# Kernel tuning notes

Hardware: AMD Instinct MI355X
Metric: run time of the kernel (lower is better)

Reference implementation:

```python
import jax, jax.numpy as jnp
import numpy as np

SIZES = [(64, 32), (32, 16), (16, 8), (8, 16), (16, 32)]
BZ, T, D = 2048, 512, 64


def setup_inputs() -> dict:
    key = jax.random.key(0)
    ks = jax.random.split(key, 32)
    inp = {
        "X": jax.random.normal(ks[0], (BZ, T, D), jnp.float32),
        "missing_mask": (jax.random.uniform(ks[1], (BZ, T, D)) < 0.8).astype(jnp.float32),
        "imputation_latent": jax.random.normal(ks[2], (BZ, T, D), jnp.float32),
    }
    for i, (din, dh) in enumerate(SIZES):
        s = 1.0 / np.sqrt(dh)  # PyTorch RNNCell init range
        k = 3 + 4 * i
        inp[f"wih{i}"] = jax.random.uniform(ks[k], (3 * dh, din), jnp.float32, -s, s)
        inp[f"whh{i}"] = jax.random.uniform(ks[k + 1], (3 * dh, dh), jnp.float32, -s, s)
        inp[f"bih{i}"] = jax.random.uniform(ks[k + 2], (3 * dh,), jnp.float32, -s, s)
        inp[f"bhh{i}"] = jax.random.uniform(ks[k + 3], (3 * dh,), jnp.float32, -s, s)
    so = 1.0 / np.sqrt(32)
    inp["out_w"] = jax.random.uniform(ks[23], (D, 32), jnp.float32, -so, so)
    inp["out_b"] = jax.random.uniform(ks[24], (D,), jnp.float32, -so, so)
    return inp


def _gru_cell(x, h, wih, whh, bih, bhh):
    # PyTorch nn.GRUCell gate order: r, z, n
    gi = x @ wih.T + bih
    gh = h @ whh.T + bhh
    ir, iz, inn = jnp.split(gi, 3, axis=-1)
    hr, hz, hn = jnp.split(gh, 3, axis=-1)
    r = jax.nn.sigmoid(ir + hr)
    z = jax.nn.sigmoid(iz + hz)
    n = jnp.tanh(inn + r * hn)
    return (1.0 - z) * n + z * h


def _forward(X, missing_mask, imputation_latent, params, out_w, out_b):
    imputed = X * missing_mask + imputation_latent * (1.0 - missing_mask)
    xs = jnp.swapaxes(imputed, 0, 1)  # [T, B, D]
    bz = X.shape[0]
    h0 = tuple(jnp.zeros((bz, dh), X.dtype) for _, dh in SIZES)

    def step(hs, x):
        new = []
        inp_x = x
        for i, (wih, whh, bih, bhh) in enumerate(params):
            h = _gru_cell(inp_x, hs[i], wih, whh, bih, bhh)
            new.append(h)
            inp_x = h  # layer i+1 consumes the freshly-updated hidden state
        return tuple(new), new[-1]

    _, hcol = jax.lax.scan(step, h0, xs)  # [T, B, 32]
    hcol = jnp.swapaxes(hcol, 0, 1)  # [B, T, 32]
    return hcol @ out_w.T + out_b


def reference(X, missing_mask, imputation_latent,
              wih0, whh0, bih0, bhh0, wih1, whh1, bih1, bhh1,
              wih2, whh2, bih2, bhh2, wih3, whh3, bih3, bhh3,
              wih4, whh4, bih4, bhh4, out_w, out_b):
    params = [(wih0, whh0, bih0, bhh0), (wih1, whh1, bih1, bhh1),
              (wih2, whh2, bih2, bhh2), (wih3, whh3, bih3, bhh3),
              (wih4, whh4, bih4, bhh4)]
    return _forward(X, missing_mask, imputation_latent, params, out_w, out_b)
```

## Files before the change

kernel.cpp:

```cpp
#include <hip/hip_runtime.h>

typedef short s16x8 __attribute__((ext_vector_type(8)));
typedef short s16x4 __attribute__((ext_vector_type(4)));
typedef float f32x4 __attribute__((ext_vector_type(4)));
typedef unsigned int u32;
typedef unsigned short u16;

#define NT 512
#define DD 64
#define BB 8
#define NTH 512

#define CHUNK 1024

#define P2STRIDE (5*CHUNK)
#define PH0 0
#define PH1 CHUNK
#define PH2 (2*CHUNK)
#define PH3 (3*CHUNK)
#define PH4 (4*CHUNK)
#define FRTOT2 (2*P2STRIDE)
#define NSTEP2 518

#define PSTRIDE (7*CHUNK)
#define XIN0 0
#define H0C (2*CHUNK)
#define H1C (3*CHUNK)
#define H2C (4*CHUNK)
#define H3C (5*CHUNK)
#define H4C (6*CHUNK)
#define FRTOT (2*PSTRIDE)
#define NSTEP_FB 517

#define MFMA16(A,B,C) __builtin_amdgcn_mfma_f32_16x16x32_bf16(A,B,C,0,0,0)

__device__ __forceinline__ float sigf(float x){ return 1.0f/(1.0f+__expf(-x)); }
__device__ __forceinline__ float tanhf2(float x){ return 2.0f/(1.0f+__expf(-2.0f*x)) - 1.0f; }

__device__ __forceinline__ u16 f2bf(float f) {
  u32 u = __builtin_bit_cast(u32, f);
  return (u16)((u + 0x7fffu + ((u >> 16) & 1u)) >> 16);
}
__device__ __forceinline__ float bf2f(u16 h) {
  u32 u = ((u32)h) << 16;
  return __builtin_bit_cast(float, u);
}

__device__ __forceinline__ void load_wfrag(const float* __restrict__ W, int row0, int nrow, int din,
                                           int kbase, int lane, s16x8& hi, s16x8& lo)
{
  const int m = lane & 15, kb = lane >> 4;
#pragma unroll
  for (int e = 0; e < 8; ++e) {
    int k = kbase + kb*8 + e;
    float v = (m < nrow && k < din) ? W[(size_t)(row0 + m)*din + k] : 0.0f;
    u16 h = f2bf(v);
    hi[e] = (short)h;
    lo[e] = (short)f2bf(v - bf2f(h));
  }
}

__device__ __forceinline__ void read_b(const u16* base, int lane, s16x8& hi, s16x8& lo)
{
  const int off = ((lane >> 4) << 8) + ((lane & 15) << 3);
  hi = *(const s16x8*)(base + off);
  lo = *(const s16x8*)(base + off + 128);
}

__device__ __forceinline__ void combine_write(
    f32x4 aR, f32x4 aZ, f32x4 aNi, f32x4 aNh,
    float (&hprev)[4], u16* hdst_base, int jbase, int nrow, int lane)
{
  const int bb = lane & 15, q = lane >> 4;
  float hv[4];
#pragma unroll
  for (int i = 0; i < 4; ++i) {
    float rr = sigf(aR[i]);
    float zz = sigf(aZ[i]);
    float nn = tanhf2(aNi[i] + rr*aNh[i]);
    hv[i] = (1.0f - zz)*nn + zz*hprev[i];
    hprev[i] = hv[i];
  }
  if (bb < 8 && q*4 < nrow) {
    const int j = jbase + q*4;
    const int kb = j >> 3, e = j & 7;
    s16x4 hh, ll;
#pragma unroll
    for (int i = 0; i < 4; ++i) {
      u16 h = f2bf(hv[i]);
      hh[i] = (short)h;
      ll[i] = (short)f2bf(hv[i] - bf2f(h));
    }
    u16* dst = hdst_base + kb*256 + bb*8 + e;
    *(s16x4*)dst = hh;
    *(s16x4*)(dst + 128) = ll;
  }
}

__global__ __launch_bounds__(256)
void gi0_gemm(const float* __restrict__ X, const float* __restrict__ M, const float* __restrict__ L,
              const float* __restrict__ wih0, const float* __restrict__ bih0,
              float* __restrict__ gi)
{
  __shared__ u32 xs[128*65];
  const int tid = threadIdx.x;
  const int wv = tid >> 6, lane = tid & 63;
  const int q = lane >> 4;
  const int b = blockIdx.x >> 2;
  const int t0 = (blockIdx.x & 3) * 128;
  const size_t base = ((size_t)b*NT + t0)*DD;

  for (int i = tid; i < 128*64; i += 256) {
    const int t = i >> 6, d = i & 63;
    float x = X[base+i], m = M[base+i], l = L[base+i];
    float v = x*m + l*(1.0f - m);
    u16 h = f2bf(v);
    u16 lo2 = f2bf(v - bf2f(h));
    xs[t*65 + d] = (u32)h | ((u32)lo2 << 16);
  }

  s16x8 Ah[6][2], Al[6][2];
  f32x4 cb[6];
#pragma unroll
  for (int tile = 0; tile < 6; ++tile) {
#pragma unroll
    for (int c = 0; c < 2; ++c)
      load_wfrag(wih0, tile*16, 16, 64, c*32, lane, Ah[tile][c], Al[tile][c]);
#pragma unroll
    for (int i = 0; i < 4; ++i) cb[tile][i] = bih0[tile*16 + q*4 + i];
  }
  __syncthreads();

#pragma unroll
  for (int g2 = 0; g2 < 2; ++g2) {
    const int tloc = g2*64 + wv*16 + (lane & 15);
    s16x8 Bh[2], Bl[2];
#pragma unroll
    for (int c = 0; c < 2; ++c) {
      const u32* p = &xs[tloc*65 + c*32 + q*8];
#pragma unroll
      for (int e = 0; e < 8; ++e) {
        u32 v = p[e];
        Bh[c][e] = (short)(v & 0xffffu);
        Bl[c][e] = (short)(v >> 16);
      }
    }
    float* gp = gi + ((size_t)b*NT + t0 + tloc)*96 + q*4;
#pragma unroll
    for (int tile = 0; tile < 6; ++tile) {
      f32x4 acc = cb[tile];
#pragma unroll
      for (int c = 0; c < 2; ++c) {
        acc = MFMA16(Ah[tile][c], Bh[c], acc);
        acc = MFMA16(Ah[tile][c], Bl[c], acc);
        acc = MFMA16(Al[tile][c], Bh[c], acc);
      }
      *(f32x4*)(gp + tile*16) = acc;
    }
  }
}

__device__ __forceinline__ void wave_l0(
    const float* __restrict__ Whh, const float* __restrict__ bhh,
    const float* __restrict__ gi, int jbase,
    u16* FRu, float* OST, float* __restrict__ out, int b0, int w, int lane)
{
  s16x8 Ahh[3], Ahl[3];
#pragma unroll
  for (int g = 0; g < 3; ++g)
    load_wfrag(Whh, g*32 + jbase, 16, 32, 0, lane, Ahh[g], Ahl[g]);
  const int q = lane >> 4;
  f32x4 cRh, cZh, cNh;
#pragma unroll
  for (int i = 0; i < 4; ++i) {
    int j = jbase + q*4 + i;
    cRh[i] = bhh[j]; cZh[i] = bhh[32+j]; cNh[i] = bhh[64+j];
  }
  float hprev[4] = {0.f,0.f,0.f,0.f};

  const size_t grow = (size_t)(b0 + (lane & 7)) * ((size_t)NT*96);
  f32x4 gR, gZ, gN;
  {
    const float* p = gi + grow + jbase + q*4;
    gR = *(const f32x4*)(p); gZ = *(const f32x4*)(p+32); gN = *(const f32x4*)(p+64);
  }
  for (int s = 0; s < NSTEP2; ++s) {
    const int par = s & 1, rp = par ^ 1;
    f32x4 nR, nZ, nN;
    if (s < 511) {
      const float* p = gi + grow + (size_t)(s+1)*96 + jbase + q*4;
      nR = *(const f32x4*)(p); nZ = *(const f32x4*)(p+32); nN = *(const f32x4*)(p+64);
    }
    if (s <= 511) {
      f32x4 aR = gR + cRh, aZ = gZ + cZh, aNi = gN, aNh = cNh;
      s16x8 bh_, bl_;
      read_b(FRu + rp*P2STRIDE + PH0, lane, bh_, bl_);
      aR  = MFMA16(Ahh[0], bh_, aR);  aR  = MFMA16(Ahh[0], bl_, aR);  aR  = MFMA16(Ahl[0], bh_, aR);
      aZ  = MFMA16(Ahh[1], bh_, aZ);  aZ  = MFMA16(Ahh[1], bl_, aZ);  aZ  = MFMA16(Ahl[1], bh_, aZ);
      aNh = MFMA16(Ahh[2], bh_, aNh); aNh = MFMA16(Ahh[2], bl_, aNh); aNh = MFMA16(Ahl[2], bh_, aNh);
      combine_write(aR, aZ, aNi, aNh, hprev, FRu + par*P2STRIDE + PH0, jbase, 16, lane);
    }
    if (s >= 6)
      out[((size_t)(b0 + w)*NT + (s-6))*DD + lane] = OST[rp*520 + w*65 + lane];
    gR = nR; gZ = nZ; gN = nN;
    __syncthreads();
  }
}

template<int DIN, int DH>
__device__ __forceinline__ void wave_mid(
    const float* __restrict__ Wih, const float* __restrict__ Whh,
    const float* __restrict__ bih, const float* __restrict__ bhh,
    int jbase, int xc, int hc, int s0, int s1,
    u16* FRu, float* OST, float* __restrict__ out, int b0, int w, int lane)
{
  const int nrow = (DH - jbase) < 16 ? (DH - jbase) : 16;
  s16x8 Axh[3], Axl[3], Ahh[3], Ahl[3];
#pragma unroll
  for (int g = 0; g < 3; ++g) {
    load_wfrag(Wih, g*DH + jbase, nrow, DIN, 0, lane, Axh[g], Axl[g]);
    load_wfrag(Whh, g*DH + jbase, nrow, DH, 0, lane, Ahh[g], Ahl[g]);
  }
  const int q = lane >> 4;
  f32x4 cR, cZ, cNi, cNh;
#pragma unroll
  for (int i = 0; i < 4; ++i) {
    int lr = q*4 + i;
    int j = jbase + lr;
    bool jr = lr < nrow;
    cR[i]  = jr ? bih[j] + bhh[j] : 0.f;
    cZ[i]  = jr ? bih[DH+j] + bhh[DH+j] : 0.f;
    cNi[i] = jr ? bih[2*DH+j] : 0.f;
    cNh[i] = jr ? bhh[2*DH+j] : 0.f;
  }
  float hprev[4] = {0.f,0.f,0.f,0.f};

  for (int s = 0; s < NSTEP2; ++s) {
    const int par = s & 1, rp = par ^ 1;
    if (s >= s0 && s <= s1) {
      f32x4 aR = cR, aZ = cZ, aNi = cNi, aNh = cNh;
      s16x8 bh_, bl_;
      read_b(FRu + rp*P2STRIDE + xc, lane, bh_, bl_);
      aR  = MFMA16(Axh[0], bh_, aR);  aR  = MFMA16(Axh[0], bl_, aR);  aR  = MFMA16(Axl[0], bh_, aR);
      aZ  = MFMA16(Axh[1], bh_, aZ);  aZ  = MFMA16(Axh[1], bl_, aZ);  aZ  = MFMA16(Axl[1], bh_, aZ);
      aNi = MFMA16(Axh[2], bh_, aNi); aNi = MFMA16(Axh[2], bl_, aNi); aNi = MFMA16(Axl[2], bh_, aNi);
      read_b(FRu + rp*P2STRIDE + hc, lane, bh_, bl_);
      aR  = MFMA16(Ahh[0], bh_, aR);  aR  = MFMA16(Ahh[0], bl_, aR);  aR  = MFMA16(Ahl[0], bh_, aR);
      aZ  = MFMA16(Ahh[1], bh_, aZ);  aZ  = MFMA16(Ahh[1], bl_, aZ);  aZ  = MFMA16(Ahl[1], bh_, aZ);
      aNh = MFMA16(Ahh[2], bh_, aNh); aNh = MFMA16(Ahh[2], bl_, aNh); aNh = MFMA16(Ahl[2], bh_, aNh);
      combine_write(aR, aZ, aNi, aNh, hprev, FRu + par*P2STRIDE + hc, jbase, nrow, lane);
    }
    if (s >= 6)
      out[((size_t)(b0 + w)*NT + (s-6))*DD + lane] = OST[rp*520 + w*65 + lane];
    __syncthreads();
  }
}

__device__ __forceinline__ void wave_out2(
    const float* __restrict__ OW, const float* __restrict__ OBb,
    u16* FRu, float* OST, float* __restrict__ out, int b0, int w, int lane)
{
  s16x8 Oh[4], Ol[4];
  f32x4 cO[4];
  const int q = lane >> 4;
#pragma unroll
  for (int t4 = 0; t4 < 4; ++t4) {
    load_wfrag(OW, t4*16, 16, 32, 0, lane, Oh[t4], Ol[t4]);
#pragma unroll
    for (int i = 0; i < 4; ++i) cO[t4][i] = OBb[t4*16 + q*4 + i];
  }
  for (int s = 0; s < NSTEP2; ++s) {
    const int par = s & 1, rp = par ^ 1;
    if (s >= 5 && s <= 516) {
      s16x8 bh_, bl_;
      read_b(FRu + rp*P2STRIDE + PH4, lane, bh_, bl_);
      const int bb = lane & 15;
#pragma unroll
      for (int t4 = 0; t4 < 4; ++t4) {
        f32x4 a_ = cO[t4];
        a_ = MFMA16(Oh[t4], bh_, a_); a_ = MFMA16(Oh[t4], bl_, a_); a_ = MFMA16(Ol[t4], bh_, a_);
        if (bb < 8) {
#pragma unroll
          for (int i = 0; i < 4; ++i) OST[par*520 + bb*65 + t4*16 + q*4 + i] = a_[i];
        }
      }
    }
    if (s >= 6)
      out[((size_t)(b0 + w)*NT + (s-6))*DD + lane] = OST[rp*520 + w*65 + lane];
    __syncthreads();
  }
}

__global__ __launch_bounds__(NTH, 1)
void gru_rec(const float* __restrict__ gi,
             const float* __restrict__ whh0, const float* __restrict__ bhh0,
             const float* __restrict__ wih1, const float* __restrict__ whh1, const float* __restrict__ bih1, const float* __restrict__ bhh1,
             const float* __restrict__ wih2, const float* __restrict__ whh2, const float* __restrict__ bih2, const float* __restrict__ bhh2,
             const float* __restrict__ wih3, const float* __restrict__ whh3, const float* __restrict__ bih3, const float* __restrict__ bhh3,
             const float* __restrict__ wih4, const float* __restrict__ whh4, const float* __restrict__ bih4, const float* __restrict__ bhh4,
             const float* __restrict__ out_w, const float* __restrict__ out_b,
             float* __restrict__ out)
{
  __shared__ __align__(16) u16 FRu[FRTOT2];
  __shared__ float OST[2*520];
  const int tid = threadIdx.x;
  const int w = tid >> 6, lane = tid & 63;
  const int b0 = blockIdx.x * BB;

  for (int i = tid; i < FRTOT2; i += NTH) FRu[i] = 0;
  for (int i = tid; i < 2*520; i += NTH) OST[i] = 0.f;
  __syncthreads();

  if (w == 0)
    wave_l0(whh0, bhh0, gi,  0, FRu, OST, out, b0, w, lane);
  else if (w == 1)
    wave_l0(whh0, bhh0, gi, 16, FRu, OST, out, b0, w, lane);
  else if (w == 2)
    wave_mid<32,16>(wih1,whh1,bih1,bhh1,  0, PH0, PH1, 1, 512, FRu, OST, out, b0, w, lane);
  else if (w == 4)
    wave_mid<16, 8>(wih2,whh2,bih2,bhh2,  0, PH1, PH2, 2, 513, FRu, OST, out, b0, w, lane);
  else if (w == 5)
    wave_mid< 8,16>(wih3,whh3,bih3,bhh3,  0, PH2, PH3, 3, 514, FRu, OST, out, b0, w, lane);
  else if (w == 3)
    wave_mid<16,32>(wih4,whh4,bih4,bhh4,  0, PH3, PH4, 4, 515, FRu, OST, out, b0, w, lane);
  else if (w == 6)
    wave_mid<16,32>(wih4,whh4,bih4,bhh4, 16, PH3, PH4, 4, 515, FRu, OST, out, b0, w, lane);
  else
    wave_out2(out_w, out_b, FRu, OST, out, b0, w, lane);
}

__device__ __forceinline__ void write_x(u16* FRu, int par, int w, int lane, float v)
{
  const int d = lane;
  const int chunk = d >> 5, kb = (d >> 3) & 3, e = d & 7;
  u16 h = f2bf(v);
  u16 l2 = f2bf(v - bf2f(h));
  u16* p = FRu + par*PSTRIDE + XIN0 + chunk*CHUNK + kb*256 + w*8 + e;
  p[0] = h; p[128] = l2;
}

template<int DIN, int DH, int NXC>
__device__ __forceinline__ void wave_gru_fb(
    const float* __restrict__ Wih, const float* __restrict__ Whh,
    const float* __restrict__ bih, const float* __restrict__ bhh,
    int jbase, int xc, int hc, int s0, int s1,
    u16* FRu, float* OST,
    const float* __restrict__ X, const float* __restrict__ Mm, const float* __restrict__ Ll,
    float* __restrict__ out, int b0, int w, int lane)
{
  const int nrow = (DH - jbase) < 16 ? (DH - jbase) : 16;
  s16x8 Axh[3][NXC], Axl[3][NXC], Ahh[3], Ahl[3];
#pragma unroll
  for (int g = 0; g < 3; ++g) {
#pragma unroll
    for (int c = 0; c < NXC; ++c)
      load_wfrag(Wih, g*DH + jbase, nrow, DIN, c*32, lane, Axh[g][c], Axl[g][c]);
    load_wfrag(Whh, g*DH + jbase, nrow, DH, 0, lane, Ahh[g], Ahl[g]);
  }
  f32x4 cR, cZ, cNi, cNh;
  {
    const int q = lane >> 4;
#pragma unroll
    for (int i = 0; i < 4; ++i) {
      int lr = q*4 + i;
      int j = jbase + lr;
      bool jr = lr < nrow;
      cR[i]  = jr ? bih[j] + bhh[j] : 0.f;
      cZ[i]  = jr ? bih[DH+j] + bhh[DH+j] : 0.f;
      cNi[i] = jr ? bih[2*DH+j] : 0.f;
      cNh[i] = jr ? bhh[2*DH+j] : 0.f;
    }
  }
  float hprev[4] = {0.f, 0.f, 0.f, 0.f};

  const size_t gbase = ((size_t)(b0 + w))*((size_t)NT*DD) + lane;
  float rx = X[gbase], rm = Mm[gbase], rl = Ll[gbase];
  write_x(FRu, 1, w, lane, rx*rm + rl*(1.0f - rm));
  rx = X[gbase + DD]; rm = Mm[gbase + DD]; rl = Ll[gbase + DD];
  __syncthreads();

  for (int s = 0; s < NSTEP_FB; ++s) {
    const int par = s & 1, rp = par ^ 1;
    float nx = 0.f, nm = 0.f, nl = 0.f;
    if (s <= 509) {
      size_t g = gbase + (size_t)(s+2)*DD;
      nx = X[g]; nm = Mm[g]; nl = Ll[g];
    }
    f32x4 aR = cR, aZ = cZ, aNi = cNi, aNh = cNh;
    const bool run = (s >= s0) && (s <= s1);
    if (run) {
      const u16* RB = FRu + rp*PSTRIDE;
      s16x8 bh_, bl_;
#pragma unroll
      for (int c = 0; c < NXC; ++c) {
        read_b(RB + xc + c*CHUNK, lane, bh_, bl_);
        aR  = MFMA16(Axh[0][c], bh_, aR);  aR  = MFMA16(Axh[0][c], bl_, aR);  aR  = MFMA16(Axl[0][c], bh_, aR);
        aZ  = MFMA16(Axh[1][c], bh_, aZ);  aZ  = MFMA16(Axh[1][c], bl_, aZ);  aZ  = MFMA16(Axl[1][c], bh_, aZ);
        aNi = MFMA16(Axh[2][c], bh_, aNi); aNi = MFMA16(Axh[2][c], bl_, aNi); aNi = MFMA16(Axl[2][c], bh_, aNi);
      }
      read_b(RB + hc, lane, bh_, bl_);
      aR  = MFMA16(Ahh[0], bh_, aR);  aR  = MFMA16(Ahh[0], bl_, aR);  aR  = MFMA16(Ahl[0], bh_, aR);
      aZ  = MFMA16(Ahh[1], bh_, aZ);  aZ  = MFMA16(Ahh[1], bl_, aZ);  aZ  = MFMA16(Ahl[1], bh_, aZ);
      aNh = MFMA16(Ahh[2], bh_, aNh); aNh = MFMA16(Ahh[2], bl_, aNh); aNh = MFMA16(Ahl[2], bh_, aNh);
    }
    __syncthreads();

    if (run)
      combine_write(aR, aZ, aNi, aNh, hprev, FRu + par*PSTRIDE + hc, jbase, nrow, lane);
    if (s >= 5)
      out[((size_t)(b0 + w)*NT + (s-5))*DD + lane] = OST[w*65 + lane];
    if (s <= 510) write_x(FRu, par, w, lane, rx*rm + rl*(1.0f - rm));
    rx = nx; rm = nm; rl = nl;
    __syncthreads();
  }
}

__device__ __forceinline__ void wave_out_fb(
    const float* __restrict__ OW, const float* __restrict__ OBb,
    u16* FRu, float* OST,
    const float* __restrict__ X, const float* __restrict__ Mm, const float* __restrict__ Ll,
    float* __restrict__ out, int b0, int w, int lane)
{
  s16x8 Oh[4], Ol[4];
  f32x4 cO[4];
#pragma unroll
  for (int t4 = 0; t4 < 4; ++t4) {
    load_wfrag(OW, t4*16, 16, 32, 0, lane, Oh[t4], Ol[t4]);
#pragma unroll
    for (int i = 0; i < 4; ++i) cO[t4][i] = OBb[t4*16 + (lane>>4)*4 + i];
  }
  const size_t gbase = ((size_t)(b0 + w))*((size_t)NT*DD) + lane;
  float rx = X[gbase], rm = Mm[gbase], rl = Ll[gbase];
  write_x(FRu, 1, w, lane, rx*rm + rl*(1.0f - rm));
  rx = X[gbase + DD]; rm = Mm[gbase + DD]; rl = Ll[gbase + DD];
  __syncthreads();

  for (int s = 0; s < NSTEP_FB; ++s) {
    const int par = s & 1, rp = par ^ 1;
    float nx = 0.f, nm = 0.f, nl = 0.f;
    if (s <= 509) { size_t g = gbase + (size_t)(s+2)*DD; nx = X[g]; nm = Mm[g]; nl = Ll[g]; }
    if (s >= 5) {
      s16x8 bh_, bl_;
      read_b(FRu + rp*PSTRIDE + H4C, lane, bh_, bl_);
      const int bb = lane & 15, q = lane >> 4;
#pragma unroll
      for (int t4 = 0; t4 < 4; ++t4) {
        f32x4 a_ = cO[t4];
        a_ = MFMA16(Oh[t4], bh_, a_); a_ = MFMA16(Oh[t4], bl_, a_); a_ = MFMA16(Ol[t4], bh_, a_);
        if (bb < 8) {
#pragma unroll
          for (int i = 0; i < 4; ++i) OST[bb*65 + t4*16 + q*4 + i] = a_[i];
        }
      }
    }
    __syncthreads();
    if (s >= 5)
      out[((size_t)(b0 + w)*NT + (s-5))*DD + lane] = OST[w*65 + lane];
    if (s <= 510) write_x(FRu, par, w, lane, rx*rm + rl*(1.0f - rm));
    rx = nx; rm = nm; rl = nl;
    __syncthreads();
  }
}

__global__ __launch_bounds__(NTH, 1)
void gru_mfma(const float* __restrict__ X, const float* __restrict__ M, const float* __restrict__ L,
              const float* __restrict__ wih0, const float* __restrict__ whh0, const float* __restrict__ bih0, const float* __restrict__ bhh0,
              const float* __restrict__ wih1, const float* __restrict__ whh1, const float* __restrict__ bih1, const float* __restrict__ bhh1,
              const float* __restrict__ wih2, const float* __restrict__ whh2, const float* __restrict__ bih2, const float* __restrict__ bhh2,
              const float* __restrict__ wih3, const float* __restrict__ whh3, const float* __restrict__ bih3, const float* __restrict__ bhh3,
              const float* __restrict__ wih4, const float* __restrict__ whh4, const float* __restrict__ bih4, const float* __restrict__ bhh4,
              const float* __restrict__ out_w, const float* __restrict__ out_b,
              float* __restrict__ out)
{
  __shared__ __align__(16) u16 FRu[FRTOT];
  __shared__ float OST[8*65];
  const int tid = threadIdx.x;
  const int w = tid >> 6, lane = tid & 63;
  const int b0 = blockIdx.x * BB;

  for (int i = tid; i < FRTOT; i += NTH) FRu[i] = 0;
  for (int i = tid; i < 8*65; i += NTH) OST[i] = 0.f;
  __syncthreads();

  if (w == 0)
    wave_gru_fb<64,32,2>(wih0,whh0,bih0,bhh0,  0, XIN0, H0C, 0, 511, FRu, OST, X,M,L, out, b0, w, lane);
  else if (w == 1)
    wave_gru_fb<64,32,2>(wih0,whh0,bih0,bhh0, 16, XIN0, H0C, 0, 511, FRu, OST, X,M,L, out, b0, w, lane);
  else if (w == 2)
    wave_gru_fb<32,16,1>(wih1,whh1,bih1,bhh1,  0, H0C,  H1C, 1, 512, FRu, OST, X,M,L, out, b0, w, lane);
  else if (w == 4)
    wave_gru_fb<16, 8,1>(wih2,whh2,bih2,bhh2,  0, H1C,  H2C, 2, 513, FRu, OST, X,M,L, out, b0, w, lane);
  else if (w == 5)
    wave_gru_fb< 8,16,1>(wih3,whh3,bih3,bhh3,  0, H2C,  H3C, 3, 514, FRu, OST, X,M,L, out, b0, w, lane);
  else if (w == 3)
    wave_gru_fb<16,32,1>(wih4,whh4,bih4,bhh4,  0, H3C,  H4C, 4, 515, FRu, OST, X,M,L, out, b0, w, lane);
  else if (w == 6)
    wave_gru_fb<16,32,1>(wih4,whh4,bih4,bhh4, 16, H3C,  H4C, 4, 515, FRu, OST, X,M,L, out, b0, w, lane);
  else
    wave_out_fb(out_w, out_b, FRu, OST, X,M,L, out, b0, w, lane);
}

extern "C" void kernel_launch(void* const* d_in, const int* in_sizes, int n_in,
                              void* d_out, int out_size, void* d_ws, size_t ws_size,
                              hipStream_t stream)
{
  const float* X  = (const float*)d_in[0];
  const float* M  = (const float*)d_in[1];
  const float* L  = (const float*)d_in[2];
  const float* wp[20];
  for (int i = 0; i < 20; ++i) wp[i] = (const float*)d_in[3 + i];
  const float* ow = (const float*)d_in[23];
  const float* ob = (const float*)d_in[24];
  float* out = (float*)d_out;

  const size_t gi_bytes = (size_t)2048 * NT * 96 * sizeof(float);
  if (ws_size >= gi_bytes) {
    float* gi = (float*)d_ws;
    gi0_gemm<<<dim3(2048*4), dim3(256), 0, stream>>>(X, M, L, wp[0], wp[2], gi);
    gru_rec<<<dim3(2048 / BB), dim3(NTH), 0, stream>>>(
        gi, wp[1], wp[3],
        wp[4], wp[5], wp[6], wp[7],
        wp[8], wp[9], wp[10], wp[11],
        wp[12], wp[13], wp[14], wp[15],
        wp[16], wp[17], wp[18], wp[19],
        ow, ob, out);
  } else {
    gru_mfma<<<dim3(2048 / BB), dim3(NTH), 0, stream>>>(
        X, M, L,
        wp[0], wp[1], wp[2], wp[3],
        wp[4], wp[5], wp[6], wp[7],
        wp[8], wp[9], wp[10], wp[11],
        wp[12], wp[13], wp[14], wp[15],
        wp[16], wp[17], wp[18], wp[19],
        ow, ob, out);
  }
}
```

Before: 976.6 us.

## Write output directly from output wave, use lighter barrier, prefetch gi two steps

The recurrent kernel's output wave now writes its MFMA results straight to global memory, so the shared OST staging buffer and the per-step copy-out that every wave did are gone. __syncthreads is replaced by a barrier that waits only on LDS counters, so global loads and stores stay in flight across steps. Layer-0 gi loads are prefetched two steps ahead, and the r/z hidden biases are folded into the gi GEMM. bf16 hi/lo splitting now uses a packed convert instruction, and the step count drops by one. The main risk is memory ordering under the weaker barrier and differences in how the packed convert rounds.

```diff
diff --git a/kernel.cpp b/kernel.cpp
--- a/kernel.cpp
+++ b/kernel.cpp
@@ -20,7 +20,7 @@
 #define PH3 (3*CHUNK)
 #define PH4 (4*CHUNK)
 #define FRTOT2 (2*P2STRIDE)
-#define NSTEP2 518
+#define NSTEP2 517
 
 #define PSTRIDE (7*CHUNK)
 #define XIN0 0
@@ -46,6 +46,18 @@
   return __builtin_bit_cast(float, u);
 }
 
+__device__ __forceinline__ void soft_barrier() {
+  asm volatile("s_waitcnt lgkmcnt(0)" ::: "memory");
+  __builtin_amdgcn_s_barrier();
+  asm volatile("" ::: "memory");
+}
+
+__device__ __forceinline__ u32 cvtpk_bf16(float a, float b) {
+  u32 r;
+  asm("v_cvt_pk_bf16_f32 %0, %1, %2" : "=v"(r) : "v"(a), "v"(b));
+  return r;
+}
+
 __device__ __forceinline__ void load_wfrag(const float* __restrict__ W, int row0, int nrow, int din,
                                            int kbase, int lane, s16x8& hi, s16x8& lo)
 {
@@ -67,7 +79,7 @@
   lo = *(const s16x8*)(base + off + 128);
 }
 
-__device__ __forceinline__ void combine_write(
+__device__ __forceinline__ void combine_write2(
     f32x4 aR, f32x4 aZ, f32x4 aNi, f32x4 aNh,
     float (&hprev)[4], u16* hdst_base, int jbase, int nrow, int lane)
 {
@@ -83,6 +95,38 @@
   }
   if (bb < 8 && q*4 < nrow) {
     const int j = jbase + q*4;
+    u16* dst = hdst_base + ((j >> 3) << 8) + bb*8 + (j & 7);
+    u32 p01 = cvtpk_bf16(hv[0], hv[1]);
+    u32 p23 = cvtpk_bf16(hv[2], hv[3]);
+    float h0 = __builtin_bit_cast(float, p01 << 16);
+    float h1 = __builtin_bit_cast(float, p01 & 0xffff0000u);
+    float h2 = __builtin_bit_cast(float, p23 << 16);
+    float h3 = __builtin_bit_cast(float, p23 & 0xffff0000u);
+    u32 q01 = cvtpk_bf16(hv[0]-h0, hv[1]-h1);
+    u32 q23 = cvtpk_bf16(hv[2]-h2, hv[3]-h3);
+    uint2 hp_; hp_.x = p01; hp_.y = p23;
+    uint2 lp_; lp_.x = q01; lp_.y = q23;
+    *(uint2*)dst = hp_;
+    *(uint2*)(dst + 128) = lp_;
+  }
+}
+
+__device__ __forceinline__ void combine_write(
+    f32x4 aR, f32x4 aZ, f32x4 aNi, f32x4 aNh,
+    float (&hprev)[4], u16* hdst_base, int jbase, int nrow, int lane)
+{
+  const int bb = lane & 15, q = lane >> 4;
+  float hv[4];
+#pragma unroll
+  for (int i = 0; i < 4; ++i) {
+    float rr = sigf(aR[i]);
+    float zz = sigf(aZ[i]);
+    float nn = tanhf2(aNi[i] + rr*aNh[i]);
+    hv[i] = (1.0f - zz)*nn + zz*hprev[i];
+    hprev[i] = hv[i];
+  }
+  if (bb < 8 && q*4 < nrow) {
+    const int j = jbase + q*4;
     const int kb = j >> 3, e = j & 7;
     s16x4 hh, ll;
 #pragma unroll
@@ -100,6 +144,7 @@
 __global__ __launch_bounds__(256)
 void gi0_gemm(const float* __restrict__ X, const float* __restrict__ M, const float* __restrict__ L,
               const float* __restrict__ wih0, const float* __restrict__ bih0,
+              const float* __restrict__ bhh0,
               float* __restrict__ gi)
 {
   __shared__ u32 xs[128*65];
@@ -111,11 +156,11 @@
   const size_t base = ((size_t)b*NT + t0)*DD;
 
   for (int i = tid; i < 128*64; i += 256) {
-    const int t = i >> 6, d = i & 63;
     float x = X[base+i], m = M[base+i], l = L[base+i];
     float v = x*m + l*(1.0f - m);
     u16 h = f2bf(v);
     u16 lo2 = f2bf(v - bf2f(h));
+    const int t = i >> 6, d = i & 63;
     xs[t*65 + d] = (u32)h | ((u32)lo2 << 16);
   }
 
@@ -127,7 +172,12 @@
     for (int c = 0; c < 2; ++c)
       load_wfrag(wih0, tile*16, 16, 64, c*32, lane, Ah[tile][c], Al[tile][c]);
 #pragma unroll
-    for (int i = 0; i < 4; ++i) cb[tile][i] = bih0[tile*16 + q*4 + i];
+    for (int i = 0; i < 4; ++i) {
+      int row = tile*16 + q*4 + i;
+      float bv = bih0[row];
+      if (tile < 4) bv += bhh0[row];
+      cb[tile][i] = bv;
+    }
   }
   __syncthreads();
 
@@ -163,47 +213,41 @@
 __device__ __forceinline__ void wave_l0(
     const float* __restrict__ Whh, const float* __restrict__ bhh,
     const float* __restrict__ gi, int jbase,
-    u16* FRu, float* OST, float* __restrict__ out, int b0, int w, int lane)
+    u16* FRu, int b0, int lane)
 {
   s16x8 Ahh[3], Ahl[3];
 #pragma unroll
   for (int g = 0; g < 3; ++g)
     load_wfrag(Whh, g*32 + jbase, 16, 32, 0, lane, Ahh[g], Ahl[g]);
   const int q = lane >> 4;
-  f32x4 cRh, cZh, cNh;
-#pragma unroll
-  for (int i = 0; i < 4; ++i) {
-    int j = jbase + q*4 + i;
-    cRh[i] = bhh[j]; cZh[i] = bhh[32+j]; cNh[i] = bhh[64+j];
-  }
+  f32x4 cNh;
+#pragma unroll
+  for (int i = 0; i < 4; ++i) cNh[i] = bhh[64 + jbase + q*4 + i];
   float hprev[4] = {0.f,0.f,0.f,0.f};
 
-  const size_t grow = (size_t)(b0 + (lane & 7)) * ((size_t)NT*96);
-  f32x4 gR, gZ, gN;
-  {
-    const float* p = gi + grow + jbase + q*4;
-    gR = *(const f32x4*)(p); gZ = *(const f32x4*)(p+32); gN = *(const f32x4*)(p+64);
-  }
+  const float* gp = gi + (size_t)(b0 + (lane & 7)) * ((size_t)NT*96) + jbase + q*4;
+  f32x4 gR0, gZ0, gN0, gR1, gZ1, gN1;
+  gR0 = *(const f32x4*)(gp); gZ0 = *(const f32x4*)(gp+32); gN0 = *(const f32x4*)(gp+64); gp += 96;
+  gR1 = *(const f32x4*)(gp); gZ1 = *(const f32x4*)(gp+32); gN1 = *(const f32x4*)(gp+64); gp += 96;
+
   for (int s = 0; s < NSTEP2; ++s) {
     const int par = s & 1, rp = par ^ 1;
-    f32x4 nR, nZ, nN;
-    if (s < 511) {
-      const float* p = gi + grow + (size_t)(s+1)*96 + jbase + q*4;
-      nR = *(const f32x4*)(p); nZ = *(const f32x4*)(p+32); nN = *(const f32x4*)(p+64);
-    }
-    if (s <= 511) {
-      f32x4 aR = gR + cRh, aZ = gZ + cZh, aNi = gN, aNh = cNh;
+    f32x4 gR2 = {}, gZ2 = {}, gN2 = {};
+    if (s + 2 < NT) {
+      gR2 = *(const f32x4*)(gp); gZ2 = *(const f32x4*)(gp+32); gN2 = *(const f32x4*)(gp+64); gp += 96;
+    }
+    if (s < NT) {
+      f32x4 aR = gR0, aZ = gZ0, aNi = gN0, aNh = cNh;
       s16x8 bh_, bl_;
       read_b(FRu + rp*P2STRIDE + PH0, lane, bh_, bl_);
       aR  = MFMA16(Ahh[0], bh_, aR);  aR  = MFMA16(Ahh[0], bl_, aR);  aR  = MFMA16(Ahl[0], bh_, aR);
       aZ  = MFMA16(Ahh[1], bh_, aZ);  aZ  = MFMA16(Ahh[1], bl_, aZ);  aZ  = MFMA16(Ahl[1], bh_, aZ);
       aNh = MFMA16(Ahh[2], bh_, aNh); aNh = MFMA16(Ahh[2], bl_, aNh); aNh = MFMA16(Ahl[2], bh_, aNh);
-      combine_write(aR, aZ, aNi, aNh, hprev, FRu + par*P2STRIDE + PH0, jbase, 16, lane);
-    }
-    if (s >= 6)
-      out[((size_t)(b0 + w)*NT + (s-6))*DD + lane] = OST[rp*520 + w*65 + lane];
-    gR = nR; gZ = nZ; gN = nN;
-    __syncthreads();
+      combine_write2(aR, aZ, aNi, aNh, hprev, FRu + par*P2STRIDE + PH0, jbase, 16, lane);
+    }
+    gR0 = gR1; gZ0 = gZ1; gN0 = gN1;
+    gR1 = gR2; gZ1 = gZ2; gN1 = gN2;
+    soft_barrier();
   }
 }
 
@@ -212,7 +256,7 @@
     const float* __restrict__ Wih, const float* __restrict__ Whh,
     const float* __restrict__ bih, const float* __restrict__ bhh,
     int jbase, int xc, int hc, int s0, int s1,
-    u16* FRu, float* OST, float* __restrict__ out, int b0, int w, int lane)
+    u16* FRu, int b0, int lane)
 {
   const int nrow = (DH - jbase) < 16 ? (DH - jbase) : 16;
   s16x8 Axh[3], Axl[3], Ahh[3], Ahl[3];
@@ -248,46 +292,41 @@
       aR  = MFMA16(Ahh[0], bh_, aR);  aR  = MFMA16(Ahh[0], bl_, aR);  aR  = MFMA16(Ahl[0], bh_, aR);
       aZ  = MFMA16(Ahh[1], bh_, aZ);  aZ  = MFMA16(Ahh[1], bl_, aZ);  aZ  = MFMA16(Ahl[1], bh_, aZ);
       aNh = MFMA16(Ahh[2], bh_, aNh); aNh = MFMA16(Ahh[2], bl_, aNh); aNh = MFMA16(Ahl[2], bh_, aNh);
-      combine_write(aR, aZ, aNi, aNh, hprev, FRu + par*P2STRIDE + hc, jbase, nrow, lane);
-    }
-    if (s >= 6)
-      out[((size_t)(b0 + w)*NT + (s-6))*DD + lane] = OST[rp*520 + w*65 + lane];
-    __syncthreads();
+      combine_write2(aR, aZ, aNi, aNh, hprev, FRu + par*P2STRIDE + hc, jbase, nrow, lane);
+    }
+    soft_barrier();
   }
 }
 
 __device__ __forceinline__ void wave_out2(
     const float* __restrict__ OW, const float* __restrict__ OBb,
-    u16* FRu, float* OST, float* __restrict__ out, int b0, int w, int lane)
+    u16* FRu, float* __restrict__ out, int b0, int lane)
 {
   s16x8 Oh[4], Ol[4];
   f32x4 cO[4];
-  const int q = lane >> 4;
+  const int q = lane >> 4, bb = lane & 15;
 #pragma unroll
   for (int t4 = 0; t4 < 4; ++t4) {
     load_wfrag(OW, t4*16, 16, 32, 0, lane, Oh[t4], Ol[t4]);
 #pragma unroll
     for (int i = 0; i < 4; ++i) cO[t4][i] = OBb[t4*16 + q*4 + i];
   }
+  float* op = out + ((size_t)(b0 + (bb & 7))*NT)*DD + q*4;
+
   for (int s = 0; s < NSTEP2; ++s) {
-    const int par = s & 1, rp = par ^ 1;
-    if (s >= 5 && s <= 516) {
+    const int rp = (s & 1) ^ 1;
+    if (s >= 5) {
       s16x8 bh_, bl_;
       read_b(FRu + rp*P2STRIDE + PH4, lane, bh_, bl_);
-      const int bb = lane & 15;
 #pragma unroll
       for (int t4 = 0; t4 < 4; ++t4) {
         f32x4 a_ = cO[t4];
         a_ = MFMA16(Oh[t4], bh_, a_); a_ = MFMA16(Oh[t4], bl_, a_); a_ = MFMA16(Ol[t4], bh_, a_);
-        if (bb < 8) {
-#pragma unroll
-          for (int i = 0; i < 4; ++i) OST[par*520 + bb*65 + t4*16 + q*4 + i] = a_[i];
-        }
+        if (bb < 8) *(f32x4*)(op + t4*16) = a_;
       }
-    }
-    if (s >= 6)
-      out[((size_t)(b0 + w)*NT + (s-6))*DD + lane] = OST[rp*520 + w*65 + lane];
-    __syncthreads();
+      op += DD;
+    }
+    soft_barrier();
   }
 }
 
@@ -302,31 +341,29 @@
              float* __restrict__ out)
 {
   __shared__ __align__(16) u16 FRu[FRTOT2];
-  __shared__ float OST[2*520];
   const int tid = threadIdx.x;
   const int w = tid >> 6, lane = tid & 63;
   const int b0 = blockIdx.x * BB;
 
   for (int i = tid; i < FRTOT2; i += NTH) FRu[i] = 0;
-  for (int i = tid; i < 2*520; i += NTH) OST[i] = 0.f;
   __syncthreads();
 
   if (w == 0)
-    wave_l0(whh0, bhh0, gi,  0, FRu, OST, out, b0, w, lane);
+    wave_l0(whh0, bhh0, gi,  0, FRu, b0, lane);
   else if (w == 1)
-    wave_l0(whh0, bhh0, gi, 16, FRu, OST, out, b0, w, lane);
+    wave_l0(whh0, bhh0, gi, 16, FRu, b0, lane);
   else if (w == 2)
-    wave_mid<32,16>(wih1,whh1,bih1,bhh1,  0, PH0, PH1, 1, 512, FRu, OST, out, b0, w, lane);
+    wave_mid<32,16>(wih1,whh1,bih1,bhh1,  0, PH0, PH1, 1, 512, FRu, b0, lane);
   else if (w == 4)
-    wave_mid<16, 8>(wih2,whh2,bih2,bhh2,  0, PH1, PH2, 2, 513, FRu, OST, out, b0, w, lane);
+    wave_mid<16, 8>(wih2,whh2,bih2,bhh2,  0, PH1, PH2, 2, 513, FRu, b0, lane);
   else if (w == 5)
-    wave_mid< 8,16>(wih3,whh3,bih3,bhh3,  0, PH2, PH3, 3, 514, FRu, OST, out, b0, w, lane);
+    wave_mid< 8,16>(wih3,whh3,bih3,bhh3,  0, PH2, PH3, 3, 514, FRu, b0, lane);
   else if (w == 3)
-    wave_mid<16,32>(wih4,whh4,bih4,bhh4,  0, PH3, PH4, 4, 515, FRu, OST, out, b0, w, lane);
+    wave_mid<16,32>(wih4,whh4,bih4,bhh4,  0, PH3, PH4, 4, 515, FRu, b0, lane);
   else if (w == 6)
-    wave_mid<16,32>(wih4,whh4,bih4,bhh4, 16, PH3, PH4, 4, 515, FRu, OST, out, b0, w, lane);
+    wave_mid<16,32>(wih4,whh4,bih4,bhh4, 16, PH3, PH4, 4, 515, FRu, b0, lane);
   else
-    wave_out2(out_w, out_b, FRu, OST, out, b0, w, lane);
+    wave_out2(out_w, out_b, FRu, out, b0, lane);
 }
 
 __device__ __forceinline__ void write_x(u16* FRu, int par, int w, int lane, float v)
@@ -516,7 +553,7 @@
   const size_t gi_bytes = (size_t)2048 * NT * 96 * sizeof(float);
   if (ws_size >= gi_bytes) {
     float* gi = (float*)d_ws;
-    gi0_gemm<<<dim3(2048*4), dim3(256), 0, stream>>>(X, M, L, wp[0], wp[2], gi);
+    gi0_gemm<<<dim3(2048*4), dim3(256), 0, stream>>>(X, M, L, wp[0], wp[2], wp[3], gi);
     gru_rec<<<dim3(2048 / BB), dim3(NTH), 0, stream>>>(
         gi, wp[1], wp[3],
         wp[4], wp[5], wp[6], wp[7],
```

Measured after the change: 840.1 us. -14.0%, faster.
